# Kernel tuning notes

Measured on AMD Instinct MI355X. Metric: run time of the kernel, lower is better.

Reference implementation:

```python
import jax, jax.numpy as jnp
import numpy as np

B, S, E, H = 2, 2048, 1024, 16
D = E // H  # head_dim = 64


def setup_inputs() -> dict:
    key = jax.random.key(0)
    ks = jax.random.split(key, 6)
    scale = 1.0 / np.sqrt(E)
    x = jax.random.normal(ks[0], (B, S, E), dtype=jnp.float32)
    mask = jnp.ones((B, S), dtype=jnp.int32)
    Wqkv = jax.random.normal(ks[1], (E, 3 * E), dtype=jnp.float32) * scale
    bqkv = jax.random.normal(ks[2], (3 * E,), dtype=jnp.float32) * 0.01
    Wout = jax.random.normal(ks[3], (E, E), dtype=jnp.float32) * scale
    bout = jax.random.normal(ks[4], (E,), dtype=jnp.float32) * 0.01
    return {"x": x, "mask": mask, "Wqkv": Wqkv, "bqkv": bqkv, "Wout": Wout, "bout": bout}


def reference(x, mask, Wqkv, bqkv, Wout, bout):
    Bn, Sn, En = x.shape
    qkv = x @ Wqkv + bqkv                      # [B,S,3E]
    qkv = qkv.reshape(Bn, Sn, 3, H, D)
    qkv = jnp.transpose(qkv, (2, 0, 3, 1, 4))  # [3,B,H,S,D]
    q, k, v = qkv[0], qkv[1], qkv[2]
    scores = jnp.einsum('bhqd,bhkd->bhqk', q, k) / np.sqrt(D).astype(np.float32)
    m = mask[:, None, None, :]                 # [B,1,1,S]
    scores = jnp.where(m == 0, jnp.float32(-jnp.inf), scores)
    attn = jax.nn.softmax(scores, axis=-1)
    out = jnp.einsum('bhqk,bhkd->bhqd', attn, v)  # [B,H,S,D]
    out = jnp.transpose(out, (0, 2, 1, 3)).reshape(Bn, Sn, En)
    return out @ Wout + bout
```

## Files before the change

### kernel.cpp

```cpp
#include <hip/hip_runtime.h>


typedef __attribute__((ext_vector_type(8))) short short8;
typedef __attribute__((ext_vector_type(4))) float floatx4;
typedef unsigned short ushort_t;

static __device__ __forceinline__ ushort_t f2bf(float f) {
    unsigned u = __float_as_uint(f);
    u += 0x7fffu + ((u >> 16) & 1u);
    return (ushort_t)(u >> 16);
}
#if __has_builtin(__builtin_amdgcn_cvt_pk_bf16_f32)
typedef __attribute__((ext_vector_type(2))) __bf16 bf16x2_t;
static __device__ __forceinline__ unsigned pack2bf(float a, float b) {
    bf16x2_t r = __builtin_amdgcn_cvt_pk_bf16_f32(a, b);
    return __builtin_bit_cast(unsigned, r);
}
#else
static __device__ __forceinline__ unsigned pack2bf(float a, float b) {
    return (unsigned)f2bf(a) | ((unsigned)f2bf(b) << 16);
}
#endif
static __device__ __forceinline__ float hexp2(float x) {
    return __builtin_amdgcn_exp2f(x);
}
static __device__ __forceinline__ void gload16(const void* g, void* l) {
    __builtin_amdgcn_global_load_lds(
        (const __attribute__((address_space(1))) unsigned int*)g,
        (__attribute__((address_space(3))) unsigned int*)l, 16, 0, 0);
}

__global__ __launch_bounds__(256) void conv_hi(const float* __restrict__ in,
                                               ushort_t* __restrict__ out) {
    int i = blockIdx.x * 256 + threadIdx.x;
    float4 v = ((const float4*)in)[i];
    uint2 o;
    o.x = pack2bf(v.x, v.y);
    o.y = pack2bf(v.z, v.w);
    ((uint2*)out)[i] = o;
}

__global__ __launch_bounds__(256) void conv_T_hi(const float* __restrict__ W,
                                                 ushort_t* __restrict__ hiT,
                                                 int K, int N) {
    __shared__ float tile[32][33];
    const int nb = blockIdx.x * 32, kb = blockIdx.y * 32;
    const int t = threadIdx.x;
    const int r = t >> 3, c4 = (t & 7) * 4;
    float4 v = *(const float4*)&W[(size_t)(kb + r) * N + nb + c4];
    tile[r][c4 + 0] = v.x; tile[r][c4 + 1] = v.y;
    tile[r][c4 + 2] = v.z; tile[r][c4 + 3] = v.w;
    __syncthreads();
    uint2 o;
    o.x = pack2bf(tile[c4 + 0][r], tile[c4 + 1][r]);
    o.y = pack2bf(tile[c4 + 2][r], tile[c4 + 3][r]);
    size_t off = ((size_t)(nb + r) * K + kb + c4) >> 2;
    ((uint2*)hiT)[off] = o;
}

__global__ __launch_bounds__(256) void transpose_v(const ushort_t* __restrict__ qkvb,
                                                   ushort_t* __restrict__ vtg) {
    __shared__ ushort_t tile[64][72];
    const int b = blockIdx.z, h = blockIdx.y, s0 = blockIdx.x * 64;
    const int t = threadIdx.x;
    #pragma unroll
    for (int p = 0; p < 2; ++p) {
        int idx = t + p * 256;
        int sl = idx >> 3, dc = (idx & 7) * 8;
        *(uint4*)&tile[sl][dc] =
            *(const uint4*)&qkvb[(size_t)(b * 2048 + s0 + sl) * 3072 + 2048 + h * 64 + dc];
    }
    __syncthreads();
    #pragma unroll
    for (int p = 0; p < 2; ++p) {
        int idx = t + p * 256;
        int dl = idx >> 3, sc = (idx & 7) * 8;
        ushort_t v[8];
        #pragma unroll
        for (int j = 0; j < 8; ++j) v[j] = tile[sc + j][dl];
        *(uint4*)&vtg[(size_t)((b * 16 + h) * 64 + dl) * 2048 + s0 + sc] = *(const uint4*)v;
    }
}

__global__ __launch_bounds__(256, 3) void gemm_bf16_bf(
    const ushort_t* __restrict__ A, const ushort_t* __restrict__ B,
    const float* __restrict__ bias, ushort_t* __restrict__ C,
    int M, int N, int K)
{
    __shared__ ushort_t Ah[128][32], Bh[128][32];
    const int bn = blockIdx.x * 128, bm = blockIdx.y * 128;
    const int t = threadIdx.x, w = t >> 6, lane = t & 63;
    const int l15 = lane & 15, quad = lane >> 4;
    const int wm = w >> 1, wn = w & 1;

    const int srow = w * 32 + (lane >> 2);
    const int skp  = (lane & 3) ^ ((lane >> 2) & 3);
    const int scol = skp * 8;
    const ushort_t* ga = A + (size_t)(bm + srow) * K + scol;
    const ushort_t* gb = B + (size_t)(bn + srow) * K + scol;
    const size_t rstep = (size_t)16 * K;
    const int fcol = ((quad ^ (l15 & 3)) * 8);

    floatx4 acc[4][4];
    #pragma unroll
    for (int mt = 0; mt < 4; ++mt)
        #pragma unroll
        for (int nt = 0; nt < 4; ++nt) acc[mt][nt] = (floatx4){0.f, 0.f, 0.f, 0.f};

    for (int k0 = 0; k0 < K; k0 += 32) {
        #pragma unroll
        for (int i = 0; i < 2; ++i) {
            gload16(ga + i * rstep + k0, &Ah[w * 32 + i * 16][0]);
            gload16(gb + i * rstep + k0, &Bh[w * 32 + i * 16][0]);
        }
        __syncthreads();
        short8 ah[4], bh[4];
        #pragma unroll
        for (int x = 0; x < 4; ++x) {
            ah[x] = *(const short8*)&Ah[wm * 64 + x * 16 + l15][fcol];
            bh[x] = *(const short8*)&Bh[wn * 64 + x * 16 + l15][fcol];
        }
        #pragma unroll
        for (int mt = 0; mt < 4; ++mt)
            #pragma unroll
            for (int nt = 0; nt < 4; ++nt)
                acc[mt][nt] = __builtin_amdgcn_mfma_f32_16x16x32_bf16(ah[mt], bh[nt], acc[mt][nt], 0, 0, 0);
        __syncthreads();
    }
    #pragma unroll
    for (int mt = 0; mt < 4; ++mt)
        #pragma unroll
        for (int r = 0; r < 4; ++r) {
            size_t row = (size_t)(bm + wm * 64 + mt * 16 + quad * 4 + r) * N;
            #pragma unroll
            for (int nt = 0; nt < 4; ++nt) {
                int col = bn + wn * 64 + nt * 16 + l15;
                C[row + col] = f2bf(acc[mt][nt][r] + bias[col]);
            }
        }
}

__global__ __launch_bounds__(256, 3) void gemm_bf16_f32(
    const ushort_t* __restrict__ A, const ushort_t* __restrict__ B,
    const float* __restrict__ bias, float* __restrict__ C,
    int M, int N, int K)
{
    __shared__ ushort_t Ah[128][32], Bh[128][32];
    const int bn = blockIdx.x * 128, bm = blockIdx.y * 128;
    const int t = threadIdx.x, w = t >> 6, lane = t & 63;
    const int l15 = lane & 15, quad = lane >> 4;
    const int wm = w >> 1, wn = w & 1;

    const int srow = w * 32 + (lane >> 2);
    const int skp  = (lane & 3) ^ ((lane >> 2) & 3);
    const int scol = skp * 8;
    const ushort_t* ga = A + (size_t)(bm + srow) * K + scol;
    const ushort_t* gb = B + (size_t)(bn + srow) * K + scol;
    const size_t rstep = (size_t)16 * K;
    const int fcol = ((quad ^ (l15 & 3)) * 8);

    floatx4 acc[4][4];
    #pragma unroll
    for (int mt = 0; mt < 4; ++mt)
        #pragma unroll
        for (int nt = 0; nt < 4; ++nt) acc[mt][nt] = (floatx4){0.f, 0.f, 0.f, 0.f};

    for (int k0 = 0; k0 < K; k0 += 32) {
        #pragma unroll
        for (int i = 0; i < 2; ++i) {
            gload16(ga + i * rstep + k0, &Ah[w * 32 + i * 16][0]);
            gload16(gb + i * rstep + k0, &Bh[w * 32 + i * 16][0]);
        }
        __syncthreads();
        short8 ah[4], bh[4];
        #pragma unroll
        for (int x = 0; x < 4; ++x) {
            ah[x] = *(const short8*)&Ah[wm * 64 + x * 16 + l15][fcol];
            bh[x] = *(const short8*)&Bh[wn * 64 + x * 16 + l15][fcol];
        }
        #pragma unroll
        for (int mt = 0; mt < 4; ++mt)
            #pragma unroll
            for (int nt = 0; nt < 4; ++nt)
                acc[mt][nt] = __builtin_amdgcn_mfma_f32_16x16x32_bf16(ah[mt], bh[nt], acc[mt][nt], 0, 0, 0);
        __syncthreads();
    }
    #pragma unroll
    for (int mt = 0; mt < 4; ++mt)
        #pragma unroll
        for (int r = 0; r < 4; ++r) {
            size_t row = (size_t)(bm + wm * 64 + mt * 16 + quad * 4 + r) * N;
            #pragma unroll
            for (int nt = 0; nt < 4; ++nt) {
                int col = bn + wn * 64 + nt * 16 + l15;
                C[row + col] = acc[mt][nt][r] + bias[col];
            }
        }
}

__global__ __launch_bounds__(256, 4) void flash_v4(
    const ushort_t* __restrict__ qkv, const ushort_t* __restrict__ vtg,
    const int* __restrict__ mask, ushort_t* __restrict__ attn, int S)
{
    __shared__ ushort_t Ks[64][64];
    __shared__ ushort_t Vt[64][64];
    __shared__ ushort_t Ps[4][16][72];
    __shared__ float Madd[64];

    const int blk = blockIdx.x;
    const int xcd = blk & 7, rr = blk >> 3;
    const int qi = rr & 31, gg = xcd + 8 * (rr >> 5);
    const int b = gg >> 4, h = gg & 15, q0 = qi * 64;

    const int t = threadIdx.x, wave = t >> 6, lane = t & 63;
    const int l15 = lane & 15, quad = lane >> 4;
    const size_t bS = (size_t)b * S;
    const float c1  = 0.125f * 1.44269504088896340736f;
    const float OFF = 24.0f;

    short8 qf[2];
    {
        int q = q0 + wave * 16 + l15;
        const ushort_t* qp = qkv + (bS + q) * 3072 + h * 64;
        qf[0] = *(const short8*)(qp + quad * 8);
        qf[1] = *(const short8*)(qp + 32 + quad * 8);
    }

    const int srow  = wave * 16 + (lane >> 3);
    const int schnk = ((lane & 7) ^ ((lane >> 3) & 7)) * 8;
    const ushort_t* gK = qkv + (bS + srow) * 3072 + 1024 + h * 64 + schnk;
    const ushort_t* gV = vtg + ((size_t)(b * 16 + h) * 64 + srow) * 2048 + schnk;

    floatx4 outacc[4];
    float lsum = 0.f;
    #pragma unroll
    for (int dt = 0; dt < 4; ++dt) outacc[dt] = (floatx4){0.f, 0.f, 0.f, 0.f};

    for (int k0 = 0; k0 < S; k0 += 64) {
        gload16(gK + (size_t)k0 * 3072,             &Ks[wave * 16][0]);
        gload16(gK + (size_t)k0 * 3072 + 8 * 3072,  &Ks[wave * 16 + 8][0]);
        gload16(gV + k0,                            &Vt[wave * 16][0]);
        gload16(gV + k0 + 8 * 2048,                 &Vt[wave * 16 + 8][0]);
        if (t < 64) Madd[t] = (mask[bS + k0 + t] ? 0.f : -1e30f) - OFF;
        __syncthreads();

        short8 kf[2][4], vf[2][4];
        #pragma unroll
        for (int kc = 0; kc < 2; ++kc)
            #pragma unroll
            for (int c = 0; c < 4; ++c) {
                int ch = ((kc * 4 + quad) ^ (l15 & 7)) * 8;
                kf[kc][c] = *(const short8*)&Ks[c * 16 + l15][ch];
                vf[kc][c] = *(const short8*)&Vt[c * 16 + l15][ch];
            }
        float4 madd4[4];
        #pragma unroll
        for (int c = 0; c < 4; ++c) madd4[c] = *(const float4*)&Madd[c * 16 + quad * 4];

        floatx4 sc[4];
        #pragma unroll
        for (int c = 0; c < 4; ++c) {
            sc[c] = (floatx4){0.f, 0.f, 0.f, 0.f};
            sc[c] = __builtin_amdgcn_mfma_f32_16x16x32_bf16(kf[0][c], qf[0], sc[c], 0, 0, 0);
            sc[c] = __builtin_amdgcn_mfma_f32_16x16x32_bf16(kf[1][c], qf[1], sc[c], 0, 0, 0);
        }
        #pragma unroll
        for (int c = 0; c < 4; ++c) {
            float p0 = hexp2(fmaf(sc[c][0], c1, madd4[c].x));
            float p1 = hexp2(fmaf(sc[c][1], c1, madd4[c].y));
            float p2 = hexp2(fmaf(sc[c][2], c1, madd4[c].z));
            float p3 = hexp2(fmaf(sc[c][3], c1, madd4[c].w));
            lsum += (p0 + p1) + (p2 + p3);
            uint2 pk;
            pk.x = pack2bf(p0, p1);
            pk.y = pack2bf(p2, p3);
            *(uint2*)&Ps[wave][l15][c * 16 + quad * 4] = pk;
        }
        short8 pf0 = *(const short8*)&Ps[wave][l15][quad * 8];
        short8 pf1 = *(const short8*)&Ps[wave][l15][32 + quad * 8];
        #pragma unroll
        for (int dt = 0; dt < 4; ++dt) {
            outacc[dt] = __builtin_amdgcn_mfma_f32_16x16x32_bf16(vf[0][dt], pf0, outacc[dt], 0, 0, 0);
            outacc[dt] = __builtin_amdgcn_mfma_f32_16x16x32_bf16(vf[1][dt], pf1, outacc[dt], 0, 0, 0);
        }
        __syncthreads();
    }

    lsum += __shfl_xor(lsum, 16);
    lsum += __shfl_xor(lsum, 32);

    {
        float inv = 1.f / lsum;
        int q = q0 + wave * 16 + l15;
        ushort_t* orow = attn + (bS + q) * 1024 + h * 64;
        #pragma unroll
        for (int dt = 0; dt < 4; ++dt) {
            uint2 pk;
            pk.x = pack2bf(outacc[dt][0] * inv, outacc[dt][1] * inv);
            pk.y = pack2bf(outacc[dt][2] * inv, outacc[dt][3] * inv);
            *(uint2*)&orow[dt * 16 + quad * 4] = pk;
        }
    }
}

extern "C" void kernel_launch(void* const* d_in, const int* in_sizes, int n_in,
                              void* d_out, int out_size, void* d_ws, size_t ws_size,
                              hipStream_t stream) {
    const float* x    = (const float*)d_in[0];
    const int*   mask = (const int*)  d_in[1];
    const float* Wqkv = (const float*)d_in[2];
    const float* bqkv = (const float*)d_in[3];
    const float* Wout = (const float*)d_in[4];
    const float* bout = (const float*)d_in[5];
    float* out = (float*)d_out;

    char* ws = (char*)d_ws;
    ushort_t* xb   = (ushort_t*)(ws);
    ushort_t* wqT  = (ushort_t*)(ws + 8388608);
    ushort_t* qkvb = (ushort_t*)(ws + 14680064);
    ushort_t* attnb= (ushort_t*)(ws + 39845888);
    ushort_t* woT  = (ushort_t*)(ws + 48234496);
    ushort_t* vtg  = (ushort_t*)(ws + 50331648);

    const int M = 4096, E = 1024, N3 = 3072, S = 2048;

    conv_hi<<<dim3(M * E / 1024), dim3(256), 0, stream>>>(x, xb);
    conv_T_hi<<<dim3(N3 / 32, E / 32), dim3(256), 0, stream>>>(Wqkv, wqT, E, N3);

    gemm_bf16_bf<<<dim3(N3 / 128, M / 128), dim3(256), 0, stream>>>(
        xb, wqT, bqkv, qkvb, M, N3, E);

    transpose_v<<<dim3(S / 64, 16, 2), dim3(256), 0, stream>>>(qkvb, vtg);

    flash_v4<<<dim3(1024), dim3(256), 0, stream>>>(qkvb, vtg, mask, attnb, S);

    conv_T_hi<<<dim3(E / 32, E / 32), dim3(256), 0, stream>>>(Wout, woT, E, E);

    gemm_bf16_f32<<<dim3(E / 128, M / 128), dim3(256), 0, stream>>>(
        attnb, woT, bout, out, M, E, E);
}
```

Baseline: 210.3 us.

## Split attention keys into two halves with combine pass; shrink output GEMM tile

The flash kernel now handles 128 queries per block, two 16-row query tiles per wave, so each K/V tile loaded into shared memory is reused twice. The key range is split into two halves handled by separate blocks, with partial outputs and row sums written to workspace. A new combine kernel merges the two halves using the normalised sum weights. The output-projection GEMM tile is reduced to 64x128 to launch more blocks. This adds an extra kernel launch and a round-trip of partial outputs through memory in exchange for better K/V reuse. The unmasked max-free softmax with a fixed offset is kept.

```diff
diff --git a/kernel.cpp b/kernel.cpp
--- a/kernel.cpp
+++ b/kernel.cpp
@@ -9,6 +9,9 @@
     unsigned u = __float_as_uint(f);
     u += 0x7fffu + ((u >> 16) & 1u);
     return (ushort_t)(u >> 16);
+}
+static __device__ __forceinline__ float bf2f(ushort_t h) {
+    return __uint_as_float(((unsigned)h) << 16);
 }
 #if __has_builtin(__builtin_amdgcn_cvt_pk_bf16_f32)
 typedef __attribute__((ext_vector_type(2))) __bf16 bf16x2_t;
@@ -140,56 +143,55 @@
         }
 }
 
-__global__ __launch_bounds__(256, 3) void gemm_bf16_f32(
+__global__ __launch_bounds__(256, 3) void gemm_bf16_f32_64(
     const ushort_t* __restrict__ A, const ushort_t* __restrict__ B,
     const float* __restrict__ bias, float* __restrict__ C,
     int M, int N, int K)
 {
-    __shared__ ushort_t Ah[128][32], Bh[128][32];
-    const int bn = blockIdx.x * 128, bm = blockIdx.y * 128;
+    __shared__ ushort_t Ah[64][32], Bh[128][32];
+    const int bn = blockIdx.x * 128, bm = blockIdx.y * 64;
     const int t = threadIdx.x, w = t >> 6, lane = t & 63;
     const int l15 = lane & 15, quad = lane >> 4;
     const int wm = w >> 1, wn = w & 1;
 
-    const int srow = w * 32 + (lane >> 2);
+    const int srow = w * 16 + (lane >> 2);
     const int skp  = (lane & 3) ^ ((lane >> 2) & 3);
     const int scol = skp * 8;
-    const ushort_t* ga = A + (size_t)(bm + srow) * K + scol;
-    const ushort_t* gb = B + (size_t)(bn + srow) * K + scol;
-    const size_t rstep = (size_t)16 * K;
+    const ushort_t* ga  = A + (size_t)(bm + srow) * K + scol;
+    const ushort_t* gb0 = B + (size_t)(bn + srow) * K + scol;
+    const ushort_t* gb1 = B + (size_t)(bn + 64 + srow) * K + scol;
     const int fcol = ((quad ^ (l15 & 3)) * 8);
 
-    floatx4 acc[4][4];
-    #pragma unroll
-    for (int mt = 0; mt < 4; ++mt)
+    floatx4 acc[2][4];
+    #pragma unroll
+    for (int mt = 0; mt < 2; ++mt)
         #pragma unroll
         for (int nt = 0; nt < 4; ++nt) acc[mt][nt] = (floatx4){0.f, 0.f, 0.f, 0.f};
 
     for (int k0 = 0; k0 < K; k0 += 32) {
-        #pragma unroll
-        for (int i = 0; i < 2; ++i) {
-            gload16(ga + i * rstep + k0, &Ah[w * 32 + i * 16][0]);
-            gload16(gb + i * rstep + k0, &Bh[w * 32 + i * 16][0]);
-        }
-        __syncthreads();
-        short8 ah[4], bh[4];
-        #pragma unroll
-        for (int x = 0; x < 4; ++x) {
-            ah[x] = *(const short8*)&Ah[wm * 64 + x * 16 + l15][fcol];
+        gload16(ga  + k0, &Ah[w * 16][0]);
+        gload16(gb0 + k0, &Bh[w * 16][0]);
+        gload16(gb1 + k0, &Bh[64 + w * 16][0]);
+        __syncthreads();
+        short8 ah[2], bh[4];
+        #pragma unroll
+        for (int x = 0; x < 2; ++x)
+            ah[x] = *(const short8*)&Ah[wm * 32 + x * 16 + l15][fcol];
+        #pragma unroll
+        for (int x = 0; x < 4; ++x)
             bh[x] = *(const short8*)&Bh[wn * 64 + x * 16 + l15][fcol];
-        }
-        #pragma unroll
-        for (int mt = 0; mt < 4; ++mt)
+        #pragma unroll
+        for (int mt = 0; mt < 2; ++mt)
             #pragma unroll
             for (int nt = 0; nt < 4; ++nt)
                 acc[mt][nt] = __builtin_amdgcn_mfma_f32_16x16x32_bf16(ah[mt], bh[nt], acc[mt][nt], 0, 0, 0);
         __syncthreads();
     }
     #pragma unroll
-    for (int mt = 0; mt < 4; ++mt)
+    for (int mt = 0; mt < 2; ++mt)
         #pragma unroll
         for (int r = 0; r < 4; ++r) {
-            size_t row = (size_t)(bm + wm * 64 + mt * 16 + quad * 4 + r) * N;
+            size_t row = (size_t)(bm + wm * 32 + mt * 16 + quad * 4 + r) * N;
             #pragma unroll
             for (int nt = 0; nt < 4; ++nt) {
                 int col = bn + wn * 64 + nt * 16 + l15;
@@ -198,9 +200,11 @@
         }
 }
 
-__global__ __launch_bounds__(256, 4) void flash_v4(
+__global__ __launch_bounds__(256, 3) void flash_v5(
     const ushort_t* __restrict__ qkv, const ushort_t* __restrict__ vtg,
-    const int* __restrict__ mask, ushort_t* __restrict__ attn, int S)
+    const int* __restrict__ mask,
+    ushort_t* __restrict__ po0, ushort_t* __restrict__ po1,
+    float* __restrict__ pl0, float* __restrict__ pl1, int S)
 {
     __shared__ ushort_t Ks[64][64];
     __shared__ ushort_t Vt[64][64];
@@ -209,8 +213,13 @@
 
     const int blk = blockIdx.x;
     const int xcd = blk & 7, rr = blk >> 3;
-    const int qi = rr & 31, gg = xcd + 8 * (rr >> 5);
-    const int b = gg >> 4, h = gg & 15, q0 = qi * 64;
+    const int qi = rr & 15, g = xcd + 8 * (rr >> 4);
+    const int half = g & 1, h = (g >> 1) & 15, b = g >> 5;
+    const int q0 = qi * 128;
+    const int kbase = half * 1024;
+
+    ushort_t* po = half ? po1 : po0;
+    float*    pl = half ? pl1 : pl0;
 
     const int t = threadIdx.x, wave = t >> 6, lane = t & 63;
     const int l15 = lane & 15, quad = lane >> 4;
@@ -218,12 +227,13 @@
     const float c1  = 0.125f * 1.44269504088896340736f;
     const float OFF = 24.0f;
 
-    short8 qf[2];
-    {
-        int q = q0 + wave * 16 + l15;
+    short8 qf[2][2];
+    #pragma unroll
+    for (int tt = 0; tt < 2; ++tt) {
+        int q = q0 + wave * 32 + tt * 16 + l15;
         const ushort_t* qp = qkv + (bS + q) * 3072 + h * 64;
-        qf[0] = *(const short8*)(qp + quad * 8);
-        qf[1] = *(const short8*)(qp + 32 + quad * 8);
+        qf[tt][0] = *(const short8*)(qp + quad * 8);
+        qf[tt][1] = *(const short8*)(qp + 32 + quad * 8);
     }
 
     const int srow  = wave * 16 + (lane >> 3);
@@ -231,12 +241,14 @@
     const ushort_t* gK = qkv + (bS + srow) * 3072 + 1024 + h * 64 + schnk;
     const ushort_t* gV = vtg + ((size_t)(b * 16 + h) * 64 + srow) * 2048 + schnk;
 
-    floatx4 outacc[4];
-    float lsum = 0.f;
-    #pragma unroll
-    for (int dt = 0; dt < 4; ++dt) outacc[dt] = (floatx4){0.f, 0.f, 0.f, 0.f};
-
-    for (int k0 = 0; k0 < S; k0 += 64) {
+    floatx4 outacc[2][4];
+    float lsum[2] = {0.f, 0.f};
+    #pragma unroll
+    for (int tt = 0; tt < 2; ++tt)
+        #pragma unroll
+        for (int dt = 0; dt < 4; ++dt) outacc[tt][dt] = (floatx4){0.f, 0.f, 0.f, 0.f};
+
+    for (int k0 = kbase; k0 < kbase + 1024; k0 += 64) {
         gload16(gK + (size_t)k0 * 3072,             &Ks[wave * 16][0]);
         gload16(gK + (size_t)k0 * 3072 + 8 * 3072,  &Ks[wave * 16 + 8][0]);
         gload16(gV + k0,                            &Vt[wave * 16][0]);
@@ -257,50 +269,78 @@
         #pragma unroll
         for (int c = 0; c < 4; ++c) madd4[c] = *(const float4*)&Madd[c * 16 + quad * 4];
 
-        floatx4 sc[4];
-        #pragma unroll
-        for (int c = 0; c < 4; ++c) {
-            sc[c] = (floatx4){0.f, 0.f, 0.f, 0.f};
-            sc[c] = __builtin_amdgcn_mfma_f32_16x16x32_bf16(kf[0][c], qf[0], sc[c], 0, 0, 0);
-            sc[c] = __builtin_amdgcn_mfma_f32_16x16x32_bf16(kf[1][c], qf[1], sc[c], 0, 0, 0);
-        }
-        #pragma unroll
-        for (int c = 0; c < 4; ++c) {
-            float p0 = hexp2(fmaf(sc[c][0], c1, madd4[c].x));
-            float p1 = hexp2(fmaf(sc[c][1], c1, madd4[c].y));
-            float p2 = hexp2(fmaf(sc[c][2], c1, madd4[c].z));
-            float p3 = hexp2(fmaf(sc[c][3], c1, madd4[c].w));
-            lsum += (p0 + p1) + (p2 + p3);
-            uint2 pk;
-            pk.x = pack2bf(p0, p1);
-            pk.y = pack2bf(p2, p3);
-            *(uint2*)&Ps[wave][l15][c * 16 + quad * 4] = pk;
-        }
-        short8 pf0 = *(const short8*)&Ps[wave][l15][quad * 8];
-        short8 pf1 = *(const short8*)&Ps[wave][l15][32 + quad * 8];
-        #pragma unroll
-        for (int dt = 0; dt < 4; ++dt) {
-            outacc[dt] = __builtin_amdgcn_mfma_f32_16x16x32_bf16(vf[0][dt], pf0, outacc[dt], 0, 0, 0);
-            outacc[dt] = __builtin_amdgcn_mfma_f32_16x16x32_bf16(vf[1][dt], pf1, outacc[dt], 0, 0, 0);
-        }
-        __syncthreads();
-    }
-
-    lsum += __shfl_xor(lsum, 16);
-    lsum += __shfl_xor(lsum, 32);
-
-    {
-        float inv = 1.f / lsum;
-        int q = q0 + wave * 16 + l15;
-        ushort_t* orow = attn + (bS + q) * 1024 + h * 64;
+        #pragma unroll
+        for (int tt = 0; tt < 2; ++tt) {
+            floatx4 sc[4];
+            #pragma unroll
+            for (int c = 0; c < 4; ++c) {
+                sc[c] = (floatx4){0.f, 0.f, 0.f, 0.f};
+                sc[c] = __builtin_amdgcn_mfma_f32_16x16x32_bf16(kf[0][c], qf[tt][0], sc[c], 0, 0, 0);
+                sc[c] = __builtin_amdgcn_mfma_f32_16x16x32_bf16(kf[1][c], qf[tt][1], sc[c], 0, 0, 0);
+            }
+            #pragma unroll
+            for (int c = 0; c < 4; ++c) {
+                float p0 = hexp2(fmaf(sc[c][0], c1, madd4[c].x));
+                float p1 = hexp2(fmaf(sc[c][1], c1, madd4[c].y));
+                float p2 = hexp2(fmaf(sc[c][2], c1, madd4[c].z));
+                float p3 = hexp2(fmaf(sc[c][3], c1, madd4[c].w));
+                lsum[tt] += (p0 + p1) + (p2 + p3);
+                uint2 pk;
+                pk.x = pack2bf(p0, p1);
+                pk.y = pack2bf(p2, p3);
+                *(uint2*)&Ps[wave][l15][c * 16 + quad * 4] = pk;
+            }
+            short8 pf0 = *(const short8*)&Ps[wave][l15][quad * 8];
+            short8 pf1 = *(const short8*)&Ps[wave][l15][32 + quad * 8];
+            #pragma unroll
+            for (int dt = 0; dt < 4; ++dt) {
+                outacc[tt][dt] = __builtin_amdgcn_mfma_f32_16x16x32_bf16(vf[0][dt], pf0, outacc[tt][dt], 0, 0, 0);
+                outacc[tt][dt] = __builtin_amdgcn_mfma_f32_16x16x32_bf16(vf[1][dt], pf1, outacc[tt][dt], 0, 0, 0);
+            }
+        }
+        __syncthreads();
+    }
+
+    #pragma unroll
+    for (int tt = 0; tt < 2; ++tt) {
+        lsum[tt] += __shfl_xor(lsum[tt], 16);
+        lsum[tt] += __shfl_xor(lsum[tt], 32);
+        lsum[tt] += 1e-30f;
+        float inv = 1.f / lsum[tt];
+        int q = q0 + wave * 32 + tt * 16 + l15;
+        ushort_t* orow = po + (bS + q) * 1024 + h * 64;
         #pragma unroll
         for (int dt = 0; dt < 4; ++dt) {
             uint2 pk;
-            pk.x = pack2bf(outacc[dt][0] * inv, outacc[dt][1] * inv);
-            pk.y = pack2bf(outacc[dt][2] * inv, outacc[dt][3] * inv);
+            pk.x = pack2bf(outacc[tt][dt][0] * inv, outacc[tt][dt][1] * inv);
+            pk.y = pack2bf(outacc[tt][dt][2] * inv, outacc[tt][dt][3] * inv);
             *(uint2*)&orow[dt * 16 + quad * 4] = pk;
         }
-    }
+        if (quad == 0) pl[(bS + q) * 16 + h] = lsum[tt];
+    }
+}
+
+__global__ __launch_bounds__(256) void combine_halves(
+    const ushort_t* __restrict__ po0, const ushort_t* __restrict__ po1,
+    const float* __restrict__ pl0, const float* __restrict__ pl1,
+    ushort_t* __restrict__ attnb)
+{
+    int i = blockIdx.x * 256 + threadIdx.x;
+    int row = i >> 8;
+    int h = (i >> 4) & 15;
+    float l0 = pl0[row * 16 + h], l1 = pl1[row * 16 + h];
+    float inv = 1.f / (l0 + l1);
+    float w0 = l0 * inv, w1 = l1 * inv;
+    uint2 a = ((const uint2*)po0)[i];
+    uint2 b2 = ((const uint2*)po1)[i];
+    float o0 = bf2f(a.x & 0xffff)  * w0 + bf2f(b2.x & 0xffff)  * w1;
+    float o1 = bf2f(a.x >> 16)     * w0 + bf2f(b2.x >> 16)     * w1;
+    float o2 = bf2f(a.y & 0xffff)  * w0 + bf2f(b2.y & 0xffff)  * w1;
+    float o3 = bf2f(a.y >> 16)     * w0 + bf2f(b2.y >> 16)     * w1;
+    uint2 o;
+    o.x = pack2bf(o0, o1);
+    o.y = pack2bf(o2, o3);
+    ((uint2*)attnb)[i] = o;
 }
 
 extern "C" void kernel_launch(void* const* d_in, const int* in_sizes, int n_in,
@@ -315,12 +355,16 @@
     float* out = (float*)d_out;
 
     char* ws = (char*)d_ws;
-    ushort_t* xb   = (ushort_t*)(ws);
-    ushort_t* wqT  = (ushort_t*)(ws + 8388608);
-    ushort_t* qkvb = (ushort_t*)(ws + 14680064);
-    ushort_t* attnb= (ushort_t*)(ws + 39845888);
-    ushort_t* woT  = (ushort_t*)(ws + 48234496);
-    ushort_t* vtg  = (ushort_t*)(ws + 50331648);
+    ushort_t* qkvb = (ushort_t*)(ws);
+    ushort_t* attnb= (ushort_t*)(ws + 25165824);
+    ushort_t* vtg  = (ushort_t*)(ws + 33554432);
+    ushort_t* woT  = (ushort_t*)(ws + 41943040);
+    ushort_t* xb   = (ushort_t*)(ws + 44040192);
+    ushort_t* wqT  = (ushort_t*)(ws + 52428800);
+    ushort_t* po0  = (ushort_t*)(ws + 44040192);
+    ushort_t* po1  = (ushort_t*)(ws + 52428800);
+    float*    pl0  = (float*)   (ws + 60817408);
+    float*    pl1  = (float*)   (ws + 61079552);
 
     const int M = 4096, E = 1024, N3 = 3072, S = 2048;
 
@@ -332,10 +376,14 @@
 
     transpose_v<<<dim3(S / 64, 16, 2), dim3(256), 0, stream>>>(qkvb, vtg);
 
-    flash_v4<<<dim3(1024), dim3(256), 0, stream>>>(qkvb, vtg, mask, attnb, S);
+    flash_v5<<<dim3(1024), dim3(256), 0, stream>>>(
+        qkvb, vtg, mask, po0, po1, pl0, pl1, S);
+
+    combine_halves<<<dim3(M * E / 4 / 256), dim3(256), 0, stream>>>(
+        po0, po1, pl0, pl1, attnb);
 
     conv_T_hi<<<dim3(E / 32, E / 32), dim3(256), 0, stream>>>(Wout, woT, E, E);
 
-    gemm_bf16_f32<<<dim3(E / 128, M / 128), dim3(256), 0, stream>>>(
+    gemm_bf16_f32_64<<<dim3(E / 128, M / 64), dim3(256), 0, stream>>>(
         attnb, woT, bout, out, M, E, E);
 }
```

New measurement: 221.5 us. +5.4%, slower.
